# Kernel tuning notes

Measured on AMD Instinct MI355X. Metric: run time of the kernel, lower is better.

Reference implementation:

```python
import jax, jax.numpy as jnp
import numpy as np

B, T, H, E = 4, 8192, 512, 2048  # batch, seq, hidden (num_dims), embed (num_embeds)
LN_EPS = 1e-5


def _layernorm(x, g, b):
    m = x.mean(-1, keepdims=True)
    v = ((x - m) ** 2).mean(-1, keepdims=True)
    return (x - m) * jax.lax.rsqrt(v + LN_EPS) * g + b


def setup_inputs() -> dict:
    key = jax.random.key(0)
    ks = jax.random.split(key, 8)
    C = 64
    tri = jnp.tril(jnp.ones((C, C), jnp.float32))
    kw = 1.0 / np.sqrt(C)
    inp = {
        "x": jax.random.normal(ks[0], (B, T, H), jnp.float32),
        "ln1_g": jnp.ones((H,), jnp.float32),
        "ln1_b": jnp.zeros((H,), jnp.float32),
        # TriLinear weights: (features, features), lower-triangular masked at init
        "W1": jax.random.uniform(ks[1], (C, C), jnp.float32, -kw, kw) * tri,
        "W2": jax.random.uniform(ks[2], (C, C), jnp.float32, -kw, kw) * tri,
        "ln2_g": jnp.ones((H,), jnp.float32),
        "ln2_b": jnp.zeros((H,), jnp.float32),
        # ffw: Linear(H->E), sin, Linear(E->H); stored (in, out)
        "fw1": jax.random.uniform(ks[3], (H, E), jnp.float32, -1.0 / np.sqrt(H), 1.0 / np.sqrt(H)),
        "fb1": jax.random.uniform(ks[4], (E,), jnp.float32, -1.0 / np.sqrt(H), 1.0 / np.sqrt(H)),
        "fw2": jax.random.uniform(ks[5], (E, H), jnp.float32, -1.0 / np.sqrt(E), 1.0 / np.sqrt(E)),
        "fb2": jax.random.uniform(ks[6], (H,), jnp.float32, -1.0 / np.sqrt(E), 1.0 / np.sqrt(E)),
        "chunk_size": 64,
        "stride": 32,
    }
    return inp


def reference(x, ln1_g, ln1_b, W1, W2, ln2_g, ln2_b, fw1, fb1, fw2, fb2, chunk_size, stride):
    Bb, Tt, Hh = x.shape
    C = chunk_size
    starts = jnp.arange(0, Tt, stride)              # (N,)
    pos = starts[:, None] + jnp.arange(C)           # (N, C)
    valid = (pos < Tt)
    vmask = valid[None, :, :, None].astype(x.dtype)
    safe = jnp.minimum(pos, Tt - 1)
    chunks = x[:, safe] * vmask                     # (B, N, C, H): padded chunks (zeros past T)
    resid = chunks
    cn = _layernorm(chunks, ln1_g, ln1_b)
    tri = jnp.tril(jnp.ones((C, C), x.dtype))
    # TriLinear on time axis (torch transposes to (B,H,C); einsum avoids the transpose)
    y = jnp.einsum('ts,bnsh->bnth', W1 * tri, cn)
    y = jnp.einsum('ts,bnsh->bnth', W2 * tri, y)
    c2 = y + resid
    h = _layernorm(c2, ln2_g, ln2_b)
    h = jnp.sin(h @ fw1 + fb1) @ fw2 + fb2
    out_chunks = (h + c2) * vmask                   # zero the padded tail (torch truncates it)
    flat = safe.reshape(-1)                         # (N*C,)
    out = jnp.zeros_like(x).at[:, flat].add(out_chunks.reshape(Bb, -1, Hh))
    counts = jnp.zeros((Tt,), x.dtype).at[flat].add(valid.reshape(-1).astype(x.dtype))
    return out / jnp.maximum(counts, 1.0)[None, :, None]
```

## Files before the change

kernel.cpp:

```cpp
#include <hip/hip_runtime.h>
#include <math.h>

#define TB 4
#define TT 8192
#define TH 512
#define TE 2048
#define NCHUNK 256
#define GCTOT 1024

typedef unsigned short u16;
typedef short bf8v __attribute__((ext_vector_type(8)));
typedef float f4v __attribute__((ext_vector_type(4)));

__device__ __forceinline__ float bu2f(u16 u) {
    unsigned int x = ((unsigned int)u) << 16; float f; __builtin_memcpy(&f, &x, 4); return f;
}
__device__ __forceinline__ u16 f2bu(float f) {
    unsigned int x; __builtin_memcpy(&x, &f, 4);
    x = x + 0x7fffu + ((x >> 16) & 1u);
    return (u16)(x >> 16);
}

__global__ __launch_bounds__(256) void make_Mt(const float* __restrict__ W1,
                                               const float* __restrict__ W2,
                                               float* __restrict__ Mt) {
    __shared__ float w1[64 * 64];
    __shared__ float w2[64 * 64];
    for (int i = threadIdx.x; i < 4096; i += 256) { w1[i] = W1[i]; w2[i] = W2[i]; }
    __syncthreads();
    for (int i = threadIdx.x; i < 4096; i += 256) {
        int t = i >> 6, s = i & 63;
        float a = 0.f;
        if (t >= s) for (int k = s; k <= t; ++k) a += w2[t * 64 + k] * w1[k * 64 + s];
        Mt[s * 64 + t] = a;
    }
}

__global__ __launch_bounds__(256) void transpose_b(const float* __restrict__ in,
                                                   u16* __restrict__ out, int R, int C) {
    __shared__ u16 tile[64][65];
    const int bx = blockIdx.x, by = blockIdx.y;
    const int tx = threadIdx.x & 63, ty = threadIdx.x >> 6;
#pragma unroll
    for (int i = 0; i < 16; ++i) {
        int r = ty + i * 4;
        tile[r][tx] = f2bu(in[(size_t)(by * 64 + r) * C + bx * 64 + tx]);
    }
    __syncthreads();
#pragma unroll
    for (int i = 0; i < 16; ++i) {
        int r = ty + i * 4;
        out[(size_t)(bx * 64 + r) * R + by * 64 + tx] = tile[tx][r];
    }
}

__global__ __launch_bounds__(256) void ln_stats(const float* __restrict__ x,
                                                float2* __restrict__ st) {
    const int wave = threadIdx.x >> 6, lane = threadIdx.x & 63;
    const size_t row = (size_t)blockIdx.x * 4 + wave;
    const float4* p = (const float4*)(x + row * TH);
    float4 a = p[lane * 2], b = p[lane * 2 + 1];
    float s = 0.f, q = 0.f;
    float v[8] = {a.x, a.y, a.z, a.w, b.x, b.y, b.z, b.w};
#pragma unroll
    for (int i = 0; i < 8; ++i) { s += v[i]; q += v[i] * v[i]; }
#pragma unroll
    for (int o = 32; o; o >>= 1) { s += __shfl_xor(s, o); q += __shfl_xor(q, o); }
    const float mean = s * (1.f / TH);
    float var = q * (1.f / TH) - mean * mean;
    if (var < 0.f) var = 0.f;
    if (lane == 0) st[row] = make_float2(mean, rsqrtf(var + 1e-5f));
}

__global__ __launch_bounds__(256) void ln_rows(const u16* __restrict__ in,
                                               u16* __restrict__ out,
                                               const float* __restrict__ g,
                                               const float* __restrict__ b) {
    const int wave = threadIdx.x >> 6, lane = threadIdx.x & 63;
    const size_t row = (size_t)blockIdx.x * 4 + wave;
    uint4 raw = *((const uint4*)(in + row * TH) + lane);
    const u16* e = (const u16*)&raw;
    float v[8]; float s = 0.f, q = 0.f;
#pragma unroll
    for (int i = 0; i < 8; ++i) { v[i] = bu2f(e[i]); s += v[i]; q += v[i] * v[i]; }
#pragma unroll
    for (int o = 32; o; o >>= 1) { s += __shfl_xor(s, o); q += __shfl_xor(q, o); }
    const float mean = s * (1.f / TH);
    float var = q * (1.f / TH) - mean * mean;
    if (var < 0.f) var = 0.f;
    const float rstd = rsqrtf(var + 1e-5f);
    float4 g0 = ((const float4*)g)[lane * 2], g1 = ((const float4*)g)[lane * 2 + 1];
    float4 b0 = ((const float4*)b)[lane * 2], b1 = ((const float4*)b)[lane * 2 + 1];
    float ge[8] = {g0.x, g0.y, g0.z, g0.w, g1.x, g1.y, g1.z, g1.w};
    float be[8] = {b0.x, b0.y, b0.z, b0.w, b1.x, b1.y, b1.z, b1.w};
    u16 ov[8];
#pragma unroll
    for (int i = 0; i < 8; ++i) ov[i] = f2bu((v[i] - mean) * rstd * ge[i] + be[i]);
    *((uint4*)(out + row * TH) + lane) = *(uint4*)ov;
}

__global__ __launch_bounds__(256) void trilinear_f(const float* __restrict__ x,
                                                   const float2* __restrict__ st,
                                                   const float* __restrict__ g,
                                                   const float* __restrict__ bb,
                                                   const float* __restrict__ Mt,
                                                   u16* __restrict__ c2s,
                                                   int gc0) {
    const int ln = blockIdx.x;
    const int gc = gc0 + ln;
    const int b = gc >> 8, n = gc & 255;
    const int h = (blockIdx.y << 8) + threadIdx.x;
    const int base = n * 32;
    const float gh = g[h], bh = bb[h];
    float acc[64];
#pragma unroll
    for (int t = 0; t < 64; ++t) acc[t] = 0.f;
    for (int s = 0; s < 64; ++s) {
        int pos = base + s; if (pos > TT - 1) pos = TT - 1;
        const size_t ro = (size_t)b * TT + pos;
        const float2 mr = st[ro];
        const float cn = (x[ro * TH + h] - mr.x) * mr.y * gh + bh;
        const float* m = Mt + s * 64;
#pragma unroll
        for (int t = 0; t < 64; ++t) acc[t] += m[t] * cn;
    }
#pragma unroll
    for (int t = 0; t < 64; ++t) {
        int pos = base + t; if (pos > TT - 1) pos = TT - 1;
        const float resid = x[((size_t)b * TT + pos) * TH + h];
        c2s[(size_t)(ln * 64 + t) * TH + h] = f2bu(acc[t] + resid);
    }
}

template <int MODE>
__global__ __launch_bounds__(512, 2) void gemm_w(const u16* __restrict__ A,
                                                 const u16* __restrict__ Bt,
                                                 u16* __restrict__ C,
                                                 const float* __restrict__ bias,
                                                 const u16* __restrict__ addp,
                                                 int N, int K) {
    __shared__ __attribute__((aligned(16))) u16 lA[2][256 * 64];
    __shared__ __attribute__((aligned(16))) u16 lB[2][256 * 64];
    const int tid = threadIdx.x;
    const int wave = tid >> 6;
    const int lane = tid & 63;
    const int wr = wave >> 2;
    const int wc = wave & 3;
    const int fr = lane & 15;
    const int fq = (lane >> 4) << 3;
    const int s8 = (fr & 7) << 3;

    int bx = blockIdx.x, by = blockIdx.y;
    const int gx = gridDim.x;
    const int nwg = gx * (int)gridDim.y;
    if ((nwg & 7) == 0) {
        const int bid = by * gx + bx;
        const int swz = (bid & 7) * (nwg >> 3) + (bid >> 3);
        bx = swz % gx; by = swz / gx;
    }
    const int bm = by << 8;
    const int bn = bx << 8;

    const int srow = tid >> 3;
    const int gch = ((tid & 7) ^ (srow & 7)) << 3;
    const u16* pa = A + (size_t)(bm + srow) * K + gch;
    const u16* pb = Bt + (size_t)(bn + srow) * K + gch;
    const int ldsw = wave << 9;

    const int NT = K >> 6;
    f4v acc[8][4] = {};

    auto stage = [&](int t, int buf) {
        const size_t ko = (size_t)t << 6;
#pragma unroll
        for (int i = 0; i < 4; ++i)
            __builtin_amdgcn_global_load_lds(
                (const __attribute__((address_space(1))) void*)(pa + (size_t)(i * 64) * K + ko),
                (__attribute__((address_space(3))) void*)(&lA[buf][(i << 12) + ldsw]), 16, 0, 0);
#pragma unroll
        for (int i = 0; i < 4; ++i)
            __builtin_amdgcn_global_load_lds(
                (const __attribute__((address_space(1))) void*)(pb + (size_t)(i * 64) * K + ko),
                (__attribute__((address_space(3))) void*)(&lB[buf][(i << 12) + ldsw]), 16, 0, 0);
    };

    stage(0, 0);
    stage(1, 1);
    asm volatile("s_waitcnt vmcnt(8)" ::: "memory");
    asm volatile("s_barrier" ::: "memory");

    const int arow0 = (wr << 7) + fr;
    const int brow0 = (wc << 6) + fr;
    const int c0 = fq ^ s8;
    const int c1 = (32 + fq) ^ s8;

    for (int t = 0; t < NT; ++t) {
        const int buf = t & 1;
        const u16* la = lA[buf];
        const u16* lb = lB[buf];
        bf8v af[8][2], bf[4][2];
#pragma unroll
        for (int mi = 0; mi < 8; ++mi) {
            af[mi][0] = *(const bf8v*)(la + ((arow0 + (mi << 4)) << 6) + c0);
            af[mi][1] = *(const bf8v*)(la + ((arow0 + (mi << 4)) << 6) + c1);
        }
#pragma unroll
        for (int ni = 0; ni < 4; ++ni) {
            bf[ni][0] = *(const bf8v*)(lb + ((brow0 + (ni << 4)) << 6) + c0);
            bf[ni][1] = *(const bf8v*)(lb + ((brow0 + (ni << 4)) << 6) + c1);
        }
        asm volatile("s_waitcnt lgkmcnt(0)" ::: "memory");
        __builtin_amdgcn_sched_barrier(0);
        asm volatile("s_barrier" ::: "memory");
        if (t + 2 < NT) stage(t + 2, buf);
        __builtin_amdgcn_s_setprio(1);
#pragma unroll
        for (int ks = 0; ks < 2; ++ks)
#pragma unroll
            for (int mi = 0; mi < 8; ++mi)
#pragma unroll
                for (int ni = 0; ni < 4; ++ni)
                    acc[mi][ni] = __builtin_amdgcn_mfma_f32_16x16x32_bf16(af[mi][ks], bf[ni][ks], acc[mi][ni], 0, 0, 0);
        __builtin_amdgcn_s_setprio(0);
        if (t + 1 < NT) {
            if (t + 2 < NT) asm volatile("s_waitcnt vmcnt(8)" ::: "memory");
            else            asm volatile("s_waitcnt vmcnt(0)" ::: "memory");
            asm volatile("s_barrier" ::: "memory");
        }
    }

    const int rq = (lane >> 4) << 2;
#pragma unroll
    for (int mi = 0; mi < 8; ++mi) {
#pragma unroll
        for (int ni = 0; ni < 4; ++ni) {
            const int col = bn + (wc << 6) + (ni << 4) + fr;
            const float bv = bias[col];
#pragma unroll
            for (int r = 0; r < 4; ++r) {
                const int row = bm + (wr << 7) + (mi << 4) + rq + r;
                float v = acc[mi][ni][r] + bv;
                if (MODE == 1) v = __sinf(v);
                else v += bu2f(addp[(size_t)row * N + col]);
                C[(size_t)row * N + col] = f2bu(v);
            }
        }
    }
}

__global__ __launch_bounds__(256) void gather_slice(const u16* __restrict__ ocs,
                                                    const u16* __restrict__ carry,
                                                    float* __restrict__ out,
                                                    int gc0) {
    const int idx = blockIdx.x * 256 + threadIdx.x;
    const int h8 = idx & 63;
    const int prow = idx >> 6;
    const int ap = gc0 * 32 + prow;
    const int b = ap >> 13, t = ap & 8191;
    const int n = t >> 5, c = t & 31;
    const int ln = (b << 8) + n - gc0;
    uint4 r1 = *((const uint4*)ocs + (size_t)(ln * 64 + c) * 64 + h8);
    const u16* e1 = (const u16*)&r1;
    float ov[8];
    if (t < 32) {
#pragma unroll
        for (int i = 0; i < 8; ++i) ov[i] = bu2f(e1[i]);
    } else {
        uint4 r0;
        if (ln == 0) r0 = *((const uint4*)carry + (size_t)(c + 32) * 64 + h8);
        else         r0 = *((const uint4*)ocs + (size_t)((ln - 1) * 64 + c + 32) * 64 + h8);
        const u16* e0 = (const u16*)&r0;
#pragma unroll
        for (int i = 0; i < 8; ++i) ov[i] = 0.5f * (bu2f(e1[i]) + bu2f(e0[i]));
    }
    float4* dst = (float4*)(out + (size_t)ap * TH + h8 * 8);
    dst[0] = make_float4(ov[0], ov[1], ov[2], ov[3]);
    dst[1] = make_float4(ov[4], ov[5], ov[6], ov[7]);
}

__global__ __launch_bounds__(256) void save_carry(const u16* __restrict__ ocs,
                                                  u16* __restrict__ carry, int SC) {
    const int i = blockIdx.x * 256 + threadIdx.x;
    ((uint4*)carry)[i] = ((const uint4*)(ocs + (size_t)(SC - 1) * 64 * TH))[i];
}

extern "C" void kernel_launch(void* const* d_in, const int* in_sizes, int n_in,
                              void* d_out, int out_size, void* d_ws, size_t ws_size,
                              hipStream_t stream) {
    const float* x   = (const float*)d_in[0];
    const float* g1  = (const float*)d_in[1];
    const float* b1  = (const float*)d_in[2];
    const float* W1  = (const float*)d_in[3];
    const float* W2  = (const float*)d_in[4];
    const float* g2  = (const float*)d_in[5];
    const float* b2  = (const float*)d_in[6];
    const float* fw1 = (const float*)d_in[7];
    const float* fb1 = (const float*)d_in[8];
    const float* fw2 = (const float*)d_in[9];
    const float* fb2 = (const float*)d_in[10];
    float* out = (float*)d_out;
    char* ws = (char*)d_ws;

    size_t o = 0;
    auto take = [&](size_t n) { size_t r = o; o = (o + n + 255) & ~(size_t)255; return r; };
    float*  Mt    = (float*) (ws + take(64 * 64 * 4));
    u16*    f1t   = (u16*)   (ws + take((size_t)TE * TH * 2));
    u16*    f2t   = (u16*)   (ws + take((size_t)TH * TE * 2));
    float2* st1   = (float2*)(ws + take((size_t)TB * TT * 8));
    u16*    carry = (u16*)   (ws + take((size_t)64 * TH * 2));
    const size_t fixed = o;

    int SC = 4;
    for (int cand = 256; cand >= 4; cand >>= 1) {
        size_t per = (size_t)cand * 64 * (TH * 2 * 3 + TE * 2) + 4 * 256;
        if (fixed + per <= ws_size) { SC = cand; break; }
    }
    u16* c2s = (u16*)(ws + take((size_t)SC * 64 * TH * 2));
    u16* h2s = (u16*)(ws + take((size_t)SC * 64 * TH * 2));
    u16* ocs = (u16*)(ws + take((size_t)SC * 64 * TH * 2));
    u16* us  = (u16*)(ws + take((size_t)SC * 64 * TE * 2));
    const int SR = SC * 64;

    make_Mt<<<1, 256, 0, stream>>>(W1, W2, Mt);
    transpose_b<<<dim3(TE / 64, TH / 64), 256, 0, stream>>>(fw1, f1t, TH, TE);
    transpose_b<<<dim3(TH / 64, TE / 64), 256, 0, stream>>>(fw2, f2t, TE, TH);
    ln_stats<<<(TB * TT) / 4, 256, 0, stream>>>(x, st1);

    for (int gc0 = 0; gc0 < GCTOT; gc0 += SC) {
        trilinear_f<<<dim3(SC, TH / 256), 256, 0, stream>>>(x, st1, g1, b1, Mt, c2s, gc0);
        ln_rows<<<SR / 4, 256, 0, stream>>>(c2s, h2s, g2, b2);
        gemm_w<1><<<dim3(TE / 256, SR / 256), 512, 0, stream>>>(
            h2s, f1t, us, fb1, (const u16*)nullptr, TE, TH);
        gemm_w<2><<<dim3(TH / 256, SR / 256), 512, 0, stream>>>(
            us, f2t, ocs, fb2, c2s, TH, TE);
        gather_slice<<<SC * 8, 256, 0, stream>>>(ocs, carry, out, gc0);
        save_carry<<<16, 256, 0, stream>>>(ocs, carry, SC);
    }
}
```

Baseline: 790.1 us.

## Use double-buffered 128x128 LDS-direct GEMM for the second FFN projection

Adds a new GEMM kernel that stages A and B tiles straight into LDS with global_load_lds into two buffers, prefetching the next K tile while MFMAs run on the current one. It also uses 128x128 tiles with 256 threads plus an XCD-aware block swizzle. It replaces the 256x256 gemm_w for the E->H projection, where N=512 gave few workgroups. The aim is better occupancy and hidden load latency, at the cost of smaller tiles and less reuse per block.

After: 692.4 us. 12.4% less time.

```diff
diff --git a/kernel.cpp b/kernel.cpp
--- a/kernel.cpp
+++ b/kernel.cpp
@@ -248,6 +248,109 @@
     }
 }
 
+template <int MODE>
+__global__ __launch_bounds__(256) void gemm_db(const u16* __restrict__ A,
+                                               const u16* __restrict__ Bt,
+                                               u16* __restrict__ C,
+                                               const float* __restrict__ bias,
+                                               const u16* __restrict__ addp,
+                                               int N, int K) {
+    __shared__ __attribute__((aligned(16))) u16 lA[2][128 * 64];
+    __shared__ __attribute__((aligned(16))) u16 lB[2][128 * 64];
+    const int tid = threadIdx.x;
+    const int wave = tid >> 6;
+    const int lane = tid & 63;
+    const int wr = wave >> 1;
+    const int wc = wave & 1;
+    const int fr = lane & 15;
+    const int fq = (lane >> 4) << 3;
+    const int s8 = (fr & 7) << 3;
+
+    int bx = blockIdx.x, by = blockIdx.y;
+    const int gx = gridDim.x;
+    const int nwg = gx * (int)gridDim.y;
+    if ((nwg & 7) == 0) {
+        const int bid = by * gx + bx;
+        const int swz = (bid & 7) * (nwg >> 3) + (bid >> 3);
+        bx = swz % gx; by = swz / gx;
+    }
+    const int bm = by << 7;
+    const int bn = bx << 7;
+
+    const int srow = tid >> 3;
+    const int gch = ((tid & 7) ^ (srow & 7)) << 3;
+    const u16* pa = A + (size_t)(bm + srow) * K + gch;
+    const u16* pb = Bt + (size_t)(bn + srow) * K + gch;
+    const int ldsw = wave << 9;
+
+    const int NT = K >> 6;
+    f4v acc[4][4] = {};
+
+    auto stage = [&](int t, int buf) {
+        const int ko = t << 6;
+#pragma unroll
+        for (int i = 0; i < 4; ++i) {
+            __builtin_amdgcn_global_load_lds(
+                (const __attribute__((address_space(1))) void*)(pa + (size_t)(i * 32) * K + ko),
+                (__attribute__((address_space(3))) void*)(&lA[buf][(i << 11) + ldsw]), 16, 0, 0);
+            __builtin_amdgcn_global_load_lds(
+                (const __attribute__((address_space(1))) void*)(pb + (size_t)(i * 32) * K + ko),
+                (__attribute__((address_space(3))) void*)(&lB[buf][(i << 11) + ldsw]), 16, 0, 0);
+        }
+    };
+
+    stage(0, 0);
+    __syncthreads();
+
+    const int arow0 = (wr << 6) + fr;
+    const int brow0 = (wc << 6) + fr;
+    const int c0 = fq ^ s8;
+    const int c1 = (32 + fq) ^ s8;
+
+    int buf = 0;
+    for (int t = 0; t < NT; ++t) {
+        if (t + 1 < NT) stage(t + 1, buf ^ 1);
+        const u16* la = lA[buf];
+        const u16* lb = lB[buf];
+#pragma unroll
+        for (int half = 0; half < 2; ++half) {
+            const int cc = half ? c1 : c0;
+            bf8v af[4], bfv[4];
+#pragma unroll
+            for (int mi = 0; mi < 4; ++mi)
+                af[mi] = *(const bf8v*)(la + ((arow0 + (mi << 4)) << 6) + cc);
+#pragma unroll
+            for (int ni = 0; ni < 4; ++ni)
+                bfv[ni] = *(const bf8v*)(lb + ((brow0 + (ni << 4)) << 6) + cc);
+#pragma unroll
+            for (int mi = 0; mi < 4; ++mi)
+#pragma unroll
+                for (int ni = 0; ni < 4; ++ni)
+                    acc[mi][ni] = __builtin_amdgcn_mfma_f32_16x16x32_bf16(af[mi], bfv[ni], acc[mi][ni], 0, 0, 0);
+        }
+        __syncthreads();
+        buf ^= 1;
+    }
+
+    const int rq = (lane >> 4) << 2;
+#pragma unroll
+    for (int mi = 0; mi < 4; ++mi) {
+#pragma unroll
+        for (int ni = 0; ni < 4; ++ni) {
+            const int col = bn + (wc << 6) + (ni << 4) + fr;
+            const float bv = bias[col];
+#pragma unroll
+            for (int r = 0; r < 4; ++r) {
+                const int row = bm + (wr << 6) + (mi << 4) + rq + r;
+                float v = acc[mi][ni][r] + bv;
+                if (MODE == 1) v = __sinf(v);
+                else v += bu2f(addp[(size_t)row * N + col]);
+                C[(size_t)row * N + col] = f2bu(v);
+            }
+        }
+    }
+}
+
 __global__ __launch_bounds__(256) void gather_slice(const u16* __restrict__ ocs,
                                                     const u16* __restrict__ carry,
                                                     float* __restrict__ out,
@@ -331,7 +434,7 @@
         ln_rows<<<SR / 4, 256, 0, stream>>>(c2s, h2s, g2, b2);
         gemm_w<1><<<dim3(TE / 256, SR / 256), 512, 0, stream>>>(
             h2s, f1t, us, fb1, (const u16*)nullptr, TE, TH);
-        gemm_w<2><<<dim3(TH / 256, SR / 256), 512, 0, stream>>>(
+        gemm_db<2><<<dim3(TH / 128, SR / 128), 256, 0, stream>>>(
             us, f2t, ocs, fb2, c2s, TH, TE);
         gather_slice<<<SC * 8, 256, 0, stream>>>(ocs, carry, out, gc0);
         save_carry<<<16, 256, 0, stream>>>(ocs, carry, SC);
```
